# Performance work log

Measured on AMD Instinct MI355X. Metric: run time of the kernel, lower is better.

Reference implementation:

```python
import jax, jax.numpy as jnp
import numpy as np
from jax import lax


def setup_inputs() -> dict:
    key = jax.random.key(0)
    k1, k2 = jax.random.split(key)
    B, H, T, F, R = 8, 16, 4096, 64, 65
    a = jax.random.normal(k1, (B, H, T, R), dtype=jnp.float32)
    v = jax.random.normal(k2, (B, H, T, F), dtype=jnp.float32)
    return {"a": a, "v": v}


def _unfold_matmul(a, v):
    # out[b,h,t,f] = sum_r a[b,h,t,r] * v[b,h, t + r - R//2, f]  (zero-padded in time)
    B, H, T, F = v.shape
    R = a.shape[-1]
    pad = R // 2
    vp = jnp.pad(v, ((0, 0), (0, 0), (pad, pad), (0, 0)))  # (B,H,T+R-1,F)

    def body(acc, r):
        vs = lax.dynamic_slice_in_dim(vp, r, T, axis=2)      # shifted values (B,H,T,F)
        ar = lax.dynamic_slice_in_dim(a, r, 1, axis=3)       # (B,H,T,1)
        return acc + ar * vs, None

    out, _ = lax.scan(body, jnp.zeros_like(v), jnp.arange(R))
    return out


def reference(a, v):
    return _unfold_matmul(a, v)
```

## Files before the change

### kernel.cpp

```cpp
#include <hip/hip_runtime.h>


#define TT 4096
#define RRR 65
#define FF 64
#define TILE 64
#define SA_S 100
#define SV_S 132
#define NTPB 4
#define RM 127

typedef short bf16x8 __attribute__((ext_vector_type(8)));
typedef float f32x16 __attribute__((ext_vector_type(16)));

__device__ __forceinline__ unsigned short f2bf(float x) {
    unsigned int u = __float_as_uint(x);
    u += 0x7fff + ((u >> 16) & 1);
    return (unsigned short)(u >> 16);
}
__device__ __forceinline__ unsigned pk2(float lo, float hi) {
    return (unsigned)f2bf(lo) | ((unsigned)f2bf(hi) << 16);
}

__global__ __launch_bounds__(256, 5)
void unfold_mfma(const float* __restrict__ a, const float* __restrict__ v,
                 float* __restrict__ out) {
    __shared__ __align__(16) unsigned short sa[TILE * SA_S];
    __shared__ __align__(16) unsigned short sv[FF * SV_S];

    const int tid = threadIdx.x;
    const int f   = tid & 63;
    const int wv  = tid >> 6;

    const int bh = blockIdx.x >> 4;
    const int T0 = (blockIdx.x & 15) << 8;

    const float* vsl = v + (size_t)bh * TT * FF;
    const size_t obase = (size_t)bh * TT * FF;

    {
        uint4 z = make_uint4(0, 0, 0, 0);
        uint4* sp = (uint4*)sa;
        #pragma unroll
        for (int it = 0; it < 4; ++it) {
            int lin = tid + it * 256;
            if (lin < (TILE * SA_S) / 8) sp[lin] = z;
        }
    }

    float4 aq[4];
    float  ae[2];
    float  vv[4][4];

    int t0 = T0;
    const float* arow = a + ((size_t)bh * TT + t0) * RRR;

#define ISSUE_A() do {                                                         \
    _Pragma("unroll")                                                          \
    for (int it = 0; it < 4; ++it) {                                           \
        int lin = tid + it * 256;                                              \
        if (lin < TILE * 15) {                                                 \
            int R = lin / 15, j = lin - R * 15;                                \
            int r0 = (4 - (R & 3)) & 3;                                        \
            aq[it] = *(const float4*)(arow + (size_t)R * RRR + r0 + 4 * j);    \
        }                                                                      \
    }                                                                          \
    _Pragma("unroll")                                                          \
    for (int it = 0; it < 2; ++it) {                                           \
        int lin = tid + it * 256;                                              \
        if (lin < TILE * 5) {                                                  \
            int R = lin / 5, e = lin - R * 5;                                  \
            int r0 = (4 - (R & 3)) & 3;                                        \
            int r = (e < r0) ? e : 60 + e;                                     \
            ae[it] = arow[(size_t)R * RRR + r];                                \
        }                                                                      \
    }                                                                          \
} while (0)

#define ISSUE_V(s0) do {                                                       \
    const int gb = (s0) + 16 * wv;                                             \
    if ((s0) + 64 <= TT) {                                                     \
        _Pragma("unroll")                                                      \
        for (int it = 0; it < 4; ++it)                                         \
            _Pragma("unroll")                                                  \
            for (int j = 0; j < 4; ++j)                                        \
                vv[it][j] = vsl[(size_t)(gb + 4 * it + j) * FF + f];           \
    } else {                                                                   \
        _Pragma("unroll")                                                      \
        for (int it = 0; it < 4; ++it)                                         \
            _Pragma("unroll")                                                  \
            for (int j = 0; j < 4; ++j) {                                      \
                int g = gb + 4 * it + j;                                       \
                vv[it][j] = (g < TT) ? vsl[(size_t)g * FF + f] : 0.f;          \
            }                                                                  \
    }                                                                          \
} while (0)

#define SCAT_A() do {                                                          \
    _Pragma("unroll")                                                          \
    for (int it = 0; it < 4; ++it) {                                           \
        int lin = tid + it * 256;                                              \
        if (lin < TILE * 15) {                                                 \
            int R = lin / 15, j = lin - R * 15;                                \
            int r0 = (4 - (R & 3)) & 3;                                        \
            int rq = r0 + 4 * j;                                               \
            float4 q = aq[it];                                                 \
            uint2 pw; pw.x = pk2(q.x, q.y); pw.y = pk2(q.z, q.w);              \
            *(uint2*)&sa[R * SA_S + (R & 31) + rq] = pw;                       \
        }                                                                      \
    }                                                                          \
    _Pragma("unroll")                                                          \
    for (int it = 0; it < 2; ++it) {                                           \
        int lin = tid + it * 256;                                              \
        if (lin < TILE * 5) {                                                  \
            int R = lin / 5, e = lin - R * 5;                                  \
            int r0 = (4 - (R & 3)) & 3;                                        \
            int r = (e < r0) ? e : 60 + e;                                     \
            sa[R * SA_S + (R & 31) + r] = f2bf(ae[it]);                        \
        }                                                                      \
    }                                                                          \
} while (0)

#define SCAT_V(s0) do {                                                        \
    const int cb = (s0) + 16 * wv;                                             \
    _Pragma("unroll")                                                          \
    for (int it = 0; it < 4; ++it) {                                           \
        uint2 pw; pw.x = pk2(vv[it][0], vv[it][1]);                            \
        pw.y = pk2(vv[it][2], vv[it][3]);                                      \
        *(uint2*)&sv[f * SV_S + ((cb + 4 * it) & RM)] = pw;                    \
    }                                                                          \
} while (0)

    ISSUE_A();
    {
        float pv[8][4];
        const int gb = T0 - 32 + 32 * wv;
        if (T0 >= 32) {
            #pragma unroll
            for (int it = 0; it < 8; ++it)
                #pragma unroll
                for (int j = 0; j < 4; ++j)
                    pv[it][j] = vsl[(size_t)(gb + 4 * it + j) * FF + f];
        } else {
            #pragma unroll
            for (int it = 0; it < 8; ++it)
                #pragma unroll
                for (int j = 0; j < 4; ++j) {
                    int g = gb + 4 * it + j;
                    pv[it][j] = (g >= 0) ? vsl[(size_t)g * FF + f] : 0.f;
                }
        }
        #pragma unroll
        for (int it = 0; it < 8; ++it) {
            uint2 pw; pw.x = pk2(pv[it][0], pv[it][1]);
            pw.y = pk2(pv[it][2], pv[it][3]);
            *(uint2*)&sv[f * SV_S + ((gb + 4 * it) & RM)] = pw;
        }
    }
    __syncthreads();

    const int n  = f & 31;
    const int hi = f >> 5;
    const int wr = wv >> 1;
    const int wc = wv & 1;
    const int Rw = 32 * wr + n;

    #pragma unroll 1
    for (int i = 0; i < NTPB; ++i) {
        SCAT_A();
        if (i > 0) SCAT_V(t0 + 32);
        const int cur_t0 = t0;
        __syncthreads();

        if (i + 1 < NTPB) {
            t0 += TILE;
            arow = a + ((size_t)bh * TT + t0) * RRR;
            ISSUE_A();
            ISSUE_V(cur_t0 + 96);
        }

        const int cbase = (cur_t0 - 32) & RM;
        f32x16 acc = {};
        #pragma unroll
        for (int kb = 0; kb < 6; ++kb) {
            const int cp = kb * 16 + hi * 8;
            bf16x8 af = *(const bf16x8*)&sa[Rw * SA_S + cp];
            bf16x8 bv = *(const bf16x8*)&sv[(32 * wc + n) * SV_S
                                            + ((cbase + 32 * wr + cp) & RM)];
            acc = __builtin_amdgcn_mfma_f32_32x32x16_bf16(af, bv, acc, 0, 0, 0);
        }

        float* op = out + obase + (size_t)(cur_t0 + 32 * wr) * FF + 32 * wc;
        #pragma unroll
        for (int reg = 0; reg < 16; ++reg) {
            int row = (reg & 3) + 8 * (reg >> 2) + 4 * hi;
            __builtin_nontemporal_store(acc[reg], &op[row * FF + n]);
        }
        __syncthreads();
    }
}

extern "C" void kernel_launch(void* const* d_in, const int* in_sizes, int n_in,
                              void* d_out, int out_size, void* d_ws, size_t ws_size,
                              hipStream_t stream) {
    const float* a = (const float*)d_in[0];
    const float* v = (const float*)d_in[1];
    float* out = (float*)d_out;

    const int BH = in_sizes[1] / (TT * FF);
    const int grid = BH * (TT / TILE) / NTPB;

    unfold_mfma<<<grid, 256, 0, stream>>>(a, v, out);
}
```

Before: 78.68 us.

## Fully unroll tile loop with double-buffered register prefetch and lightweight barriers

Replaces the 4-iteration tile loop with an unrolled sequence that keeps two register sets of prefetched a/v data, so global loads for a tile are issued two tiles ahead instead of one. It also swaps __syncthreads for a custom barrier that only waits on LDS counters, so outstanding global loads are not drained at each barrier. This costs extra registers, which may reduce occupancy under the launch bounds.

```diff
diff --git a/kernel.cpp b/kernel.cpp
--- a/kernel.cpp
+++ b/kernel.cpp
@@ -22,6 +22,13 @@
     return (unsigned)f2bf(lo) | ((unsigned)f2bf(hi) << 16);
 }
 
+#define BAR() do {                                                             \
+    asm volatile("s_waitcnt lgkmcnt(0)" ::: "memory");                         \
+    __builtin_amdgcn_sched_barrier(0);                                         \
+    __builtin_amdgcn_s_barrier();                                              \
+    __builtin_amdgcn_sched_barrier(0);                                         \
+} while (0)
+
 __global__ __launch_bounds__(256, 5)
 void unfold_mfma(const float* __restrict__ a, const float* __restrict__ v,
                  float* __restrict__ out) {
@@ -31,6 +38,11 @@
     const int tid = threadIdx.x;
     const int f   = tid & 63;
     const int wv  = tid >> 6;
+    const int n   = f & 31;
+    const int hi  = f >> 5;
+    const int wr  = wv >> 1;
+    const int wc  = wv & 1;
+    const int Rw  = 32 * wr + n;
 
     const int bh = blockIdx.x >> 4;
     const int T0 = (blockIdx.x & 15) << 8;
@@ -48,21 +60,15 @@
         }
     }
 
-    float4 aq[4];
-    float  ae[2];
-    float  vv[4][4];
-
-    int t0 = T0;
-    const float* arow = a + ((size_t)bh * TT + t0) * RRR;
-
-#define ISSUE_A() do {                                                         \
+#define ISSUE_A_(AQ, AE, TROW) do {                                            \
+    const float* arow_ = a + ((size_t)bh * TT + (TROW)) * RRR;                 \
     _Pragma("unroll")                                                          \
     for (int it = 0; it < 4; ++it) {                                           \
         int lin = tid + it * 256;                                              \
         if (lin < TILE * 15) {                                                 \
             int R = lin / 15, j = lin - R * 15;                                \
             int r0 = (4 - (R & 3)) & 3;                                        \
-            aq[it] = *(const float4*)(arow + (size_t)R * RRR + r0 + 4 * j);    \
+            AQ[it] = *(const float4*)(arow_ + (size_t)R * RRR + r0 + 4 * j);   \
         }                                                                      \
     }                                                                          \
     _Pragma("unroll")                                                          \
@@ -72,31 +78,31 @@
             int R = lin / 5, e = lin - R * 5;                                  \
             int r0 = (4 - (R & 3)) & 3;                                        \
             int r = (e < r0) ? e : 60 + e;                                     \
-            ae[it] = arow[(size_t)R * RRR + r];                                \
-        }                                                                      \
-    }                                                                          \
-} while (0)
-
-#define ISSUE_V(s0) do {                                                       \
-    const int gb = (s0) + 16 * wv;                                             \
-    if ((s0) + 64 <= TT) {                                                     \
+            AE[it] = arow_[(size_t)R * RRR + r];                               \
+        }                                                                      \
+    }                                                                          \
+} while (0)
+
+#define ISSUE_V_(VV, S0) do {                                                  \
+    const int gb_ = (S0) + 16 * wv;                                            \
+    if ((S0) + 64 <= TT) {                                                     \
         _Pragma("unroll")                                                      \
         for (int it = 0; it < 4; ++it)                                         \
             _Pragma("unroll")                                                  \
             for (int j = 0; j < 4; ++j)                                        \
-                vv[it][j] = vsl[(size_t)(gb + 4 * it + j) * FF + f];           \
+                VV[it][j] = vsl[(size_t)(gb_ + 4 * it + j) * FF + f];          \
     } else {                                                                   \
         _Pragma("unroll")                                                      \
         for (int it = 0; it < 4; ++it)                                         \
             _Pragma("unroll")                                                  \
             for (int j = 0; j < 4; ++j) {                                      \
-                int g = gb + 4 * it + j;                                       \
-                vv[it][j] = (g < TT) ? vsl[(size_t)g * FF + f] : 0.f;          \
+                int g = gb_ + 4 * it + j;                                      \
+                VV[it][j] = (g < TT) ? vsl[(size_t)g * FF + f] : 0.f;          \
             }                                                                  \
     }                                                                          \
 } while (0)
 
-#define SCAT_A() do {                                                          \
+#define SCAT_A_(AQ, AE) do {                                                   \
     _Pragma("unroll")                                                          \
     for (int it = 0; it < 4; ++it) {                                           \
         int lin = tid + it * 256;                                              \
@@ -104,7 +110,7 @@
             int R = lin / 15, j = lin - R * 15;                                \
             int r0 = (4 - (R & 3)) & 3;                                        \
             int rq = r0 + 4 * j;                                               \
-            float4 q = aq[it];                                                 \
+            float4 q = AQ[it];                                                 \
             uint2 pw; pw.x = pk2(q.x, q.y); pw.y = pk2(q.z, q.w);              \
             *(uint2*)&sa[R * SA_S + (R & 31) + rq] = pw;                       \
         }                                                                      \
@@ -116,22 +122,45 @@
             int R = lin / 5, e = lin - R * 5;                                  \
             int r0 = (4 - (R & 3)) & 3;                                        \
             int r = (e < r0) ? e : 60 + e;                                     \
-            sa[R * SA_S + (R & 31) + r] = f2bf(ae[it]);                        \
-        }                                                                      \
-    }                                                                          \
-} while (0)
-
-#define SCAT_V(s0) do {                                                        \
-    const int cb = (s0) + 16 * wv;                                             \
+            sa[R * SA_S + (R & 31) + r] = f2bf(AE[it]);                        \
+        }                                                                      \
+    }                                                                          \
+} while (0)
+
+#define SCAT_V_(VV, S0) do {                                                   \
+    const int cb_ = (S0) + 16 * wv;                                            \
     _Pragma("unroll")                                                          \
     for (int it = 0; it < 4; ++it) {                                           \
-        uint2 pw; pw.x = pk2(vv[it][0], vv[it][1]);                            \
-        pw.y = pk2(vv[it][2], vv[it][3]);                                      \
-        *(uint2*)&sv[f * SV_S + ((cb + 4 * it) & RM)] = pw;                    \
-    }                                                                          \
-} while (0)
-
-    ISSUE_A();
+        uint2 pw; pw.x = pk2(VV[it][0], VV[it][1]);                            \
+        pw.y = pk2(VV[it][2], VV[it][3]);                                      \
+        *(uint2*)&sv[f * SV_S + ((cb_ + 4 * it) & RM)] = pw;                   \
+    }                                                                          \
+} while (0)
+
+#define COMPUTE_(TROW) do {                                                    \
+    const int cbase_ = ((TROW) - 32) & RM;                                     \
+    f32x16 acc = {};                                                           \
+    _Pragma("unroll")                                                          \
+    for (int kb = 0; kb < 6; ++kb) {                                           \
+        const int cp = kb * 16 + hi * 8;                                       \
+        bf16x8 af = *(const bf16x8*)&sa[Rw * SA_S + cp];                       \
+        bf16x8 bv = *(const bf16x8*)&sv[(32 * wc + n) * SV_S                   \
+                                        + ((cbase_ + 32 * wr + cp) & RM)];     \
+        acc = __builtin_amdgcn_mfma_f32_32x32x16_bf16(af, bv, acc, 0, 0, 0);   \
+    }                                                                          \
+    float* op = out + obase + (size_t)((TROW) + 32 * wr) * FF + 32 * wc;       \
+    _Pragma("unroll")                                                          \
+    for (int reg = 0; reg < 16; ++reg) {                                       \
+        int row = (reg & 3) + 8 * (reg >> 2) + 4 * hi;                         \
+        __builtin_nontemporal_store(acc[reg], &op[row * FF + n]);              \
+    }                                                                          \
+} while (0)
+
+    float4 aqA[4], aqB[4];
+    float  aeA[2], aeB[2];
+    float  vvA[4][4], vvB[4][4];
+
+    ISSUE_A_(aqA, aeA, T0);
     {
         float pv[8][4];
         const int gb = T0 - 32 + 32 * wv;
@@ -157,47 +186,35 @@
             *(uint2*)&sv[f * SV_S + ((gb + 4 * it) & RM)] = pw;
         }
     }
-    __syncthreads();
-
-    const int n  = f & 31;
-    const int hi = f >> 5;
-    const int wr = wv >> 1;
-    const int wc = wv & 1;
-    const int Rw = 32 * wr + n;
-
-    #pragma unroll 1
-    for (int i = 0; i < NTPB; ++i) {
-        SCAT_A();
-        if (i > 0) SCAT_V(t0 + 32);
-        const int cur_t0 = t0;
-        __syncthreads();
-
-        if (i + 1 < NTPB) {
-            t0 += TILE;
-            arow = a + ((size_t)bh * TT + t0) * RRR;
-            ISSUE_A();
-            ISSUE_V(cur_t0 + 96);
-        }
-
-        const int cbase = (cur_t0 - 32) & RM;
-        f32x16 acc = {};
-        #pragma unroll
-        for (int kb = 0; kb < 6; ++kb) {
-            const int cp = kb * 16 + hi * 8;
-            bf16x8 af = *(const bf16x8*)&sa[Rw * SA_S + cp];
-            bf16x8 bv = *(const bf16x8*)&sv[(32 * wc + n) * SV_S
-                                            + ((cbase + 32 * wr + cp) & RM)];
-            acc = __builtin_amdgcn_mfma_f32_32x32x16_bf16(af, bv, acc, 0, 0, 0);
-        }
-
-        float* op = out + obase + (size_t)(cur_t0 + 32 * wr) * FF + 32 * wc;
-        #pragma unroll
-        for (int reg = 0; reg < 16; ++reg) {
-            int row = (reg & 3) + 8 * (reg >> 2) + 4 * hi;
-            __builtin_nontemporal_store(acc[reg], &op[row * FF + n]);
-        }
-        __syncthreads();
-    }
+    ISSUE_A_(aqB, aeB, T0 + 64);
+    ISSUE_V_(vvB, T0 + 96);
+    BAR();
+
+    SCAT_A_(aqA, aeA);
+    BAR();
+    ISSUE_A_(aqA, aeA, T0 + 128);
+    ISSUE_V_(vvA, T0 + 160);
+    COMPUTE_(T0);
+    BAR();
+
+    SCAT_A_(aqB, aeB);
+    SCAT_V_(vvB, T0 + 96);
+    BAR();
+    ISSUE_A_(aqB, aeB, T0 + 192);
+    ISSUE_V_(vvB, T0 + 224);
+    COMPUTE_(T0 + 64);
+    BAR();
+
+    SCAT_A_(aqA, aeA);
+    SCAT_V_(vvA, T0 + 160);
+    BAR();
+    COMPUTE_(T0 + 128);
+    BAR();
+
+    SCAT_A_(aqB, aeB);
+    SCAT_V_(vvB, T0 + 224);
+    BAR();
+    COMPUTE_(T0 + 192);
 }
 
 extern "C" void kernel_launch(void* const* d_in, const int* in_sizes, int n_in,
```

Measured after the change: 287.1 us. 3.65x slower.
